# Performance work log

Hardware: AMD Instinct MI355X
Metric: run time of the kernel (lower is better)

The kernel has to match this reference:

```python
import jax, jax.numpy as jnp
import numpy as np

B, S, D_MODEL = 1, 2048, 2048
N_HEADS, N_KV_HEADS, D_HEAD = 16, 4, 128
ROTARY_DIM, ROTARY_BASE = 128, 10000.0
ATTN_SCALE = float(np.sqrt(D_HEAD))
REPEAT = N_HEADS // N_KV_HEADS


def _sin_cos_rotary(n_ctx, rotary_dim, base):
    # TransformerLens calculate_sin_cos_rotary, rotary_adjacent_pairs=False:
    # freq repeated as 'd -> (2 d)'
    pos = jnp.arange(n_ctx, dtype=jnp.float32)
    dim = jnp.arange(rotary_dim // 2, dtype=jnp.float32)
    freq = base ** (dim / (rotary_dim / 2))
    freq = jnp.concatenate([freq, freq])  # (2 d)
    angles = pos[:, None] / freq[None, :]  # [n_ctx, rotary_dim]
    return jnp.sin(angles), jnp.cos(angles)


def _rotate_every_two_half(x):
    # rotate_half for non-adjacent pairs: [-x2, x1]
    d = x.shape[-1]
    return jnp.concatenate([-x[..., d // 2:], x[..., : d // 2]], axis=-1)


def _apply_rotary(x, sin, cos):
    # x: [batch, pos, head, d_head]; sin/cos: [n_ctx, rotary_dim]
    p = x.shape[1]
    s = sin[:p][:, None, :]  # [pos, 1, rotary_dim]
    c = cos[:p][:, None, :]
    x_rot = x[..., :ROTARY_DIM]
    x_pass = x[..., ROTARY_DIM:]
    x_rotated = x_rot * c + _rotate_every_two_half(x_rot) * s
    return jnp.concatenate([x_rotated, x_pass], axis=-1)


def setup_inputs() -> dict:
    key = jax.random.key(0)
    ks = jax.random.split(key, 10)
    init = 1.0 / np.sqrt(D_MODEL)
    return {
        "query_input": jax.random.normal(ks[0], (B, S, D_MODEL), jnp.float32),
        "key_input": jax.random.normal(ks[1], (B, S, D_MODEL), jnp.float32),
        "value_input": jax.random.normal(ks[2], (B, S, D_MODEL), jnp.float32),
        "W_Q": jax.random.normal(ks[3], (N_HEADS, D_MODEL, D_HEAD), jnp.float32) * init,
        "b_Q": jnp.zeros((N_HEADS, D_HEAD), jnp.float32),
        "W_K": jax.random.normal(ks[4], (N_KV_HEADS, D_MODEL, D_HEAD), jnp.float32) * init,
        "b_K": jnp.zeros((N_KV_HEADS, D_HEAD), jnp.float32),
        "W_V": jax.random.normal(ks[5], (N_KV_HEADS, D_MODEL, D_HEAD), jnp.float32) * init,
        "b_V": jnp.zeros((N_KV_HEADS, D_HEAD), jnp.float32),
        "W_O": jax.random.normal(ks[6], (N_HEADS, D_HEAD, D_MODEL), jnp.float32) * init,
        "b_O": jnp.zeros((D_MODEL,), jnp.float32),
    }


def reference(query_input, key_input, value_input, W_Q, b_Q, W_K, b_K, W_V, b_V, W_O, b_O):
    sin, cos = _sin_cos_rotary(S, ROTARY_DIM, ROTARY_BASE)

    # Projections
    q = jnp.einsum("bpd,hdk->bphk", query_input, W_Q) + b_Q   # [B,S,H,dh]
    k = jnp.einsum("bpd,hdk->bphk", key_input, W_K) + b_K     # [B,S,Hkv,dh]
    v = jnp.einsum("bpd,hdk->bphk", value_input, W_V) + b_V   # [B,S,Hkv,dh]

    # Rotary on q and k (before KV head expansion)
    q = _apply_rotary(q, sin, cos)
    k = _apply_rotary(k, sin, cos)

    # GQA expansion via repeat_interleave on head dim
    k = jnp.repeat(k, REPEAT, axis=2)  # [B,S,H,dh]
    v = jnp.repeat(v, REPEAT, axis=2)

    # Attention scores, causal mask, softmax
    scores = jnp.einsum("bqhd,bkhd->bhqk", q, k) / ATTN_SCALE  # [B,H,S,S]
    causal = jnp.tril(jnp.ones((S, S), dtype=bool))
    scores = jnp.where(causal, scores, jnp.finfo(scores.dtype).min)
    pattern = jax.nn.softmax(scores, axis=-1)

    # Weighted values and output projection
    z = jnp.einsum("bhqk,bkhd->bqhd", pattern, v)              # [B,S,H,dh]
    out = jnp.einsum("bqhd,hdm->bqm", z, W_O) + b_O            # [B,S,D]
    return out
```

## Files before the change

### kernel.cpp

```cpp
#include <hip/hip_runtime.h>
#include <hip/hip_bf16.h>
#include <stdint.h>
#include <math.h>

typedef __bf16 bf16_t;
typedef __attribute__((ext_vector_type(8))) __bf16 bf16x8;
typedef __attribute__((ext_vector_type(4))) __bf16 bf16x4;
typedef __attribute__((ext_vector_type(4))) float f32x4;
typedef __attribute__((ext_vector_type(16))) float f32x16;
typedef unsigned int uint2v __attribute__((ext_vector_type(2)));

static constexpr int S = 2048;
static constexpr int DM = 2048;
static constexpr int NH = 16;
static constexpr int NKV = 4;
static constexpr int DH = 128;

#define MFMA16(a, b, c) __builtin_amdgcn_mfma_f32_16x16x32_bf16((a), (b), (c), 0, 0, 0)
#define MFMA32(a, b, c) __builtin_amdgcn_mfma_f32_32x32x16_bf16((a), (b), (c), 0, 0, 0)

__device__ __forceinline__ void gload_lds16(const void* g, void* l) {
  __builtin_amdgcn_global_load_lds((__attribute__((address_space(1))) void*)(g),
                                   (__attribute__((address_space(3))) void*)(l), 16, 0, 0);
}

template <int N>
__device__ __forceinline__ void wait_vmcnt() {
  asm volatile("s_waitcnt vmcnt(%0)" :: "n"(N) : "memory");
}
__device__ __forceinline__ void wait_lgkm0() {
  asm volatile("s_waitcnt lgkmcnt(0)" ::: "memory");
}

__device__ __forceinline__ unsigned cvtpk(float lo, float hi) {
  unsigned r;
  asm("v_cvt_pk_bf16_f32 %0, %1, %2" : "=v"(r) : "v"(lo), "v"(hi));
  return r;
}
__device__ __forceinline__ void plswap2(unsigned& a, unsigned& b) {
  uint2v r = __builtin_amdgcn_permlane32_swap(a, b, false, false);
  a = r[0]; b = r[1];
}
__device__ __forceinline__ float swapred_max(float x) {
  uint2v r = __builtin_amdgcn_permlane32_swap(__float_as_uint(x), __float_as_uint(x), false, false);
  return fmaxf(__uint_as_float(r[0]), __uint_as_float(r[1]));
}
__device__ __forceinline__ float swapred_sum(float x) {
  uint2v r = __builtin_amdgcn_permlane32_swap(__float_as_uint(x), __float_as_uint(x), false, false);
  return __uint_as_float(r[0]) + __uint_as_float(r[1]);
}
__device__ __forceinline__ bf16x8 packfrag(float a0, float a1, float a2, float a3,
                                           float a4, float a5, float a6, float a7) {
  unsigned w0 = cvtpk(a0, a1), w1 = cvtpk(a2, a3);
  unsigned w2 = cvtpk(a4, a5), w3 = cvtpk(a6, a7);
  plswap2(w0, w2); plswap2(w1, w3);
  union { unsigned u[4]; bf16x8 v; } u;
  u.u[0] = w0; u.u[1] = w1; u.u[2] = w2; u.u[3] = w3;
  return u.v;
}

__device__ const unsigned char attn_map[24] = {
  (15<<1)|0,(15<<1)|1,(7<<1)|0,(14<<1)|0,(14<<1)|1,(13<<1)|0,(13<<1)|1,(6<<1)|0,
  (12<<1)|0,(12<<1)|1,(5<<1)|0,(11<<1)|0,(11<<1)|1,(10<<1)|0,(10<<1)|1,(9<<1)|0,
  (9<<1)|1,(4<<1)|0,(8<<1)|0,(8<<1)|1,(3<<1)|0,(2<<1)|0,(1<<1)|0,(0<<1)|0};

__global__ void rope_table_k(float2* __restrict__ tab) {
  int p = blockIdx.x;
  int j = threadIdx.x;
  double inv = exp2(-(double)j * 13.287712379549449 / 64.0);
  double ang = (double)p * inv;
  tab[p * 64 + j] = make_float2((float)sin(ang), (float)cos(ang));
}

__global__ void cvt3_k(const float* __restrict__ Xq, const float* __restrict__ Xk,
                       const float* __restrict__ Xv, bf16_t* __restrict__ xq,
                       bf16_t* __restrict__ xk, bf16_t* __restrict__ xv) {
  int i = (blockIdx.x * 256 + threadIdx.x) * 4;
  const float* in; bf16_t* out; int off;
  if (i < 4194304) { in = Xq; out = xq; off = i; }
  else if (i < 8388608) { in = Xk; out = xk; off = i - 4194304; }
  else { in = Xv; out = xv; off = i - 8388608; }
  f32x4 v = *(const f32x4*)(in + off);
  bf16x4 o;
  o[0] = (bf16_t)v[0]; o[1] = (bf16_t)v[1]; o[2] = (bf16_t)v[2]; o[3] = (bf16_t)v[3];
  *(bf16x4*)(out + off) = o;
}

__global__ void transpose_w_k(const float* __restrict__ in, bf16_t* __restrict__ out,
                              int R, int C, int rb, int cb, int ldo) {
  __shared__ float tile[32][33];
  int b = blockIdx.z;
  int c0 = blockIdx.x * 32, r0 = blockIdx.y * 32;
  int tx = threadIdx.x, ty = threadIdx.y;
  const float* src = in + (size_t)b * R * C;
  #pragma unroll
  for (int j = 0; j < 32; j += 8)
    tile[ty + j][tx] = src[(size_t)(r0 + ty + j) * C + c0 + tx];
  __syncthreads();
  #pragma unroll
  for (int j = 0; j < 32; j += 8) {
    int c = c0 + ty + j;
    int r = r0 + tx;
    out[(size_t)(b * rb + c) * ldo + b * cb + r] = (bf16_t)tile[tx][ty + j];
  }
}

__global__ void transpose_wkv_k(const float* __restrict__ WK, const float* __restrict__ WV,
                                bf16_t* __restrict__ wkT, bf16_t* __restrict__ wvT) {
  __shared__ float tile[32][33];
  int z = blockIdx.z;
  int b = z & 3;
  const float* in = (z < 4) ? WK : WV;
  bf16_t* out = (z < 4) ? wkT : wvT;
  int c0 = blockIdx.x * 32, r0 = blockIdx.y * 32;
  int tx = threadIdx.x, ty = threadIdx.y;
  const float* src = in + (size_t)b * 2048 * 128;
  #pragma unroll
  for (int j = 0; j < 32; j += 8)
    tile[ty + j][tx] = src[(size_t)(r0 + ty + j) * 128 + c0 + tx];
  __syncthreads();
  #pragma unroll
  for (int j = 0; j < 32; j += 8) {
    int c = c0 + ty + j;
    int r = r0 + tx;
    out[(size_t)(b * 128 + c) * 2048 + r] = (bf16_t)tile[tx][ty + j];
  }
}

__global__ void rope_qk_k(bf16_t* __restrict__ Qb, bf16_t* __restrict__ Kb,
                          const float2* __restrict__ tab, float qscale) {
  int tid = blockIdx.x * 256 + threadIdx.x;
  int row = tid >> 4;
  int i = (tid & 15) * 4;
  bf16_t* base; float scale;
  if (row < NH * S) { base = Qb + (size_t)row * DH; scale = qscale; }
  else { base = Kb + (size_t)(row - NH * S) * DH; scale = 1.0f; }
  int p = row & (S - 1);
  bf16x4 lo = *(bf16x4*)(base + i);
  bf16x4 hi = *(bf16x4*)(base + i + 64);
  float4 t0 = *(const float4*)(tab + p * 64 + i);
  float4 t1 = *(const float4*)(tab + p * 64 + i + 2);
  float sv[4] = {t0.x, t0.z, t1.x, t1.z};
  float cv[4] = {t0.y, t0.w, t1.y, t1.w};
  bf16x4 nlo, nhi;
  #pragma unroll
  for (int j = 0; j < 4; ++j) {
    float a = (float)lo[j], b = (float)hi[j];
    nlo[j] = (bf16_t)((a * cv[j] - b * sv[j]) * scale);
    nhi[j] = (bf16_t)((b * cv[j] + a * sv[j]) * scale);
  }
  *(bf16x4*)(base + i) = nlo;
  *(bf16x4*)(base + i + 64) = nhi;
}

__global__ __launch_bounds__(256)
void proj_gemm_k(const bf16_t* __restrict__ xq, const bf16_t* __restrict__ xk,
                 const bf16_t* __restrict__ xv, const bf16_t* __restrict__ wqT,
                 const bf16_t* __restrict__ wkT, const bf16_t* __restrict__ wvT,
                 const float* __restrict__ bQ, const float* __restrict__ bK,
                 const float* __restrict__ bV, bf16_t* __restrict__ Qb,
                 bf16_t* __restrict__ Kb, bf16_t* __restrict__ Vt) {
  const int nb = blockIdx.x;
  const int m0 = blockIdx.y * 128;
  const bf16_t* A; const bf16_t* B; const float* bias; bf16_t* dst; int ncol0;
  bool vmode = false;
  if (nb < 32)      { A = xq; B = wqT; bias = bQ; dst = Qb; ncol0 = nb * 64; }
  else if (nb < 40) { A = xk; B = wkT; bias = bK; dst = Kb; ncol0 = (nb - 32) * 64; }
  else              { A = xv; B = wvT; bias = bV; dst = Vt; ncol0 = (nb - 40) * 64; vmode = true; }
  const int K = 2048;
  const int t = threadIdx.x;
  const int lane = t & 63, w = t >> 6;
  const int l15 = lane & 15, lg = lane >> 4;
  const int wr = (w >> 1) * 64, wc = (w & 1) * 32;

  __shared__ bf16_t lA[2][128 * 64];
  __shared__ bf16_t lB[2][64 * 64];

  f32x4 acc[4][2] = {};
  const int srow = t >> 3;
  const int sslot = t & 7;

  auto stage = [&](int buf, int kt) {
    #pragma unroll
    for (int i = 0; i < 4; ++i) {
      int row = i * 32 + srow;
      int ss = sslot ^ (row & 7);
      gload_lds16(A + (size_t)(m0 + row) * K + kt * 64 + ss * 8,
                  (void*)(&lA[buf][0] + i * 2048 + t * 8));
    }
    #pragma unroll
    for (int i = 0; i < 2; ++i) {
      int row = i * 32 + srow;
      int ss = sslot ^ (row & 7);
      gload_lds16(B + (size_t)(ncol0 + row) * K + kt * 64 + ss * 8,
                  (void*)(&lB[buf][0] + i * 2048 + t * 8));
    }
  };

  const int nk = K >> 6;
  stage(0, 0);
  for (int kt = 0; kt < nk; ++kt) {
    const int cur = kt & 1;
    if (kt + 1 < nk) {
      stage(cur ^ 1, kt + 1);
      wait_vmcnt<6>();
    } else {
      wait_vmcnt<0>();
    }
    __builtin_amdgcn_s_barrier();
    #pragma unroll
    for (int kk = 0; kk < 2; ++kk) {
      bf16x8 af[4], bfv[2];
      #pragma unroll
      for (int f = 0; f < 4; ++f) {
        int row = wr + f * 16 + l15;
        int slot = kk * 4 + lg;
        af[f] = *(const bf16x8*)(&lA[cur][0] + row * 64 + ((slot ^ (row & 7)) * 8));
      }
      #pragma unroll
      for (int f = 0; f < 2; ++f) {
        int row = wc + f * 16 + l15;
        int slot = kk * 4 + lg;
        bfv[f] = *(const bf16x8*)(&lB[cur][0] + row * 64 + ((slot ^ (row & 7)) * 8));
      }
      #pragma unroll
      for (int fm = 0; fm < 4; ++fm)
        #pragma unroll
        for (int fn = 0; fn < 2; ++fn)
          acc[fm][fn] = MFMA16(af[fm], bfv[fn], acc[fm][fn]);
    }
    wait_lgkm0();
    __builtin_amdgcn_s_barrier();
  }

  #pragma unroll
  for (int fm = 0; fm < 4; ++fm) {
    int rowb = m0 + wr + fm * 16 + lg * 4;
    #pragma unroll
    for (int fn = 0; fn < 2; ++fn) {
      int col = ncol0 + wc + fn * 16 + l15;
      float bb = bias[col];
      if (vmode) {
        bf16x4 pk;
        #pragma unroll
        for (int r = 0; r < 4; ++r) pk[r] = (bf16_t)(acc[fm][fn][r] + bb);
        *(bf16x4*)(dst + (size_t)col * S + rowb) = pk;
      } else {
        #pragma unroll
        for (int r = 0; r < 4; ++r) {
          float v = acc[fm][fn][r] + bb;
          dst[((size_t)(col >> 7) * S + (rowb + r)) * DH + (col & 127)] = (bf16_t)v;
        }
      }
    }
  }
}

__global__ __launch_bounds__(256)
void gemm_o_k(const bf16_t* __restrict__ A, const bf16_t* __restrict__ B,
              const float* __restrict__ bias, float* __restrict__ Cout) {
  const int ncol0 = blockIdx.x * 64;
  const int m0 = blockIdx.y * 128;
  const int K = 2048;
  const int t = threadIdx.x;
  const int lane = t & 63, w = t >> 6;
  const int l15 = lane & 15, lg = lane >> 4;
  const int wr = (w >> 1) * 64, wc = (w & 1) * 32;

  __shared__ bf16_t lA[2][128 * 64];
  __shared__ bf16_t lB[2][64 * 64];

  f32x4 acc[4][2] = {};
  const int srow = t >> 3;
  const int sslot = t & 7;

  auto stage = [&](int buf, int kt) {
    #pragma unroll
    for (int i = 0; i < 4; ++i) {
      int row = i * 32 + srow;
      int ss = sslot ^ (row & 7);
      gload_lds16(A + (size_t)(m0 + row) * K + kt * 64 + ss * 8,
                  (void*)(&lA[buf][0] + i * 2048 + t * 8));
    }
    #pragma unroll
    for (int i = 0; i < 2; ++i) {
      int row = i * 32 + srow;
      int ss = sslot ^ (row & 7);
      gload_lds16(B + (size_t)(ncol0 + row) * K + kt * 64 + ss * 8,
                  (void*)(&lB[buf][0] + i * 2048 + t * 8));
    }
  };

  const int nk = K >> 6;
  stage(0, 0);
  for (int kt = 0; kt < nk; ++kt) {
    const int cur = kt & 1;
    if (kt + 1 < nk) {
      stage(cur ^ 1, kt + 1);
      wait_vmcnt<6>();
    } else {
      wait_vmcnt<0>();
    }
    __builtin_amdgcn_s_barrier();
    #pragma unroll
    for (int kk = 0; kk < 2; ++kk) {
      bf16x8 af[4], bfv[2];
      #pragma unroll
      for (int f = 0; f < 4; ++f) {
        int row = wr + f * 16 + l15;
        int slot = kk * 4 + lg;
        af[f] = *(const bf16x8*)(&lA[cur][0] + row * 64 + ((slot ^ (row & 7)) * 8));
      }
      #pragma unroll
      for (int f = 0; f < 2; ++f) {
        int row = wc + f * 16 + l15;
        int slot = kk * 4 + lg;
        bfv[f] = *(const bf16x8*)(&lB[cur][0] + row * 64 + ((slot ^ (row & 7)) * 8));
      }
      #pragma unroll
      for (int fm = 0; fm < 4; ++fm)
        #pragma unroll
        for (int fn = 0; fn < 2; ++fn)
          acc[fm][fn] = MFMA16(af[fm], bfv[fn], acc[fm][fn]);
    }
    wait_lgkm0();
    __builtin_amdgcn_s_barrier();
  }

  #pragma unroll
  for (int fm = 0; fm < 4; ++fm) {
    int rowb = m0 + wr + fm * 16 + lg * 4;
    #pragma unroll
    for (int fn = 0; fn < 2; ++fn) {
      int col = ncol0 + wc + fn * 16 + l15;
      float bb = bias[col];
      #pragma unroll
      for (int r = 0; r < 4; ++r)
        Cout[(size_t)(rowb + r) * DM + col] = acc[fm][fn][r] + bb;
    }
  }
}

__global__ __launch_bounds__(256, 2)
void attn_k(const bf16_t* __restrict__ Q, const bf16_t* __restrict__ K,
            const bf16_t* __restrict__ Vt, bf16_t* __restrict__ Z,
            float* __restrict__ Opart, float* __restrict__ mpart,
            float* __restrict__ lpart) {
  const int bid = blockIdx.x;
  const int h = bid & 15;
  const int g = bid >> 4;
  const int code = attn_map[g];
  const int qb = code >> 1, ci = code & 1;
  const bool split = qb >= 8;
  const int kt0 = (split && ci) ? (qb + 1) : 0;
  const int ktend = split ? (ci ? 2 * qb + 1 : qb) : 2 * qb + 1;
  const int q0 = qb * 128;
  const int hkv = h >> 2;
  const int t = threadIdx.x;
  const int lane = t & 63, w = t >> 6;
  const int l31 = lane & 31, hi = lane >> 5;
  const int qrow = q0 + w * 32 + l31;

  __shared__ bf16_t lK[2][64 * 128];
  __shared__ bf16_t lV[2][128 * 64];

  bf16x8 qf[8];
  #pragma unroll
  for (int j = 0; j < 8; ++j)
    qf[j] = *(const bf16x8*)(Q + ((size_t)h * S + qrow) * DH + j * 16 + hi * 8);

  auto stageKV = [&](int buf, int kt) {
    #pragma unroll
    for (int i = 0; i < 4; ++i) {
      int row = i * 16 + (t >> 4);
      int ss = (t & 15) ^ (row & 15);
      gload_lds16(K + ((size_t)hkv * S + kt * 64 + row) * DH + ss * 8,
                  (void*)(&lK[buf][0] + i * 2048 + t * 8));
    }
    #pragma unroll
    for (int i = 0; i < 4; ++i) {
      int row = i * 32 + (t >> 3);
      int ss = (t & 7) ^ (row & 7);
      gload_lds16(Vt + ((size_t)hkv * DH + row) * S + kt * 64 + ss * 8,
                  (void*)(&lV[buf][0] + i * 2048 + t * 8));
    }
  };

  f32x16 oacc0 = {}, oacc1 = {}, oacc2 = {}, oacc3 = {};
  float m_run = -3.0e3f, l_run = 0.f;

  stageKV(0, kt0);
  for (int kt = kt0; kt <= ktend; ++kt) {
    const int cur = (kt - kt0) & 1;
    if (kt < ktend) {
      stageKV(cur ^ 1, kt + 1);
      wait_vmcnt<8>();
    } else {
      wait_vmcnt<0>();
    }
    __builtin_amdgcn_s_barrier();

    f32x16 s0 = {}, s1 = {};
    __builtin_amdgcn_s_setprio(1);
    #pragma unroll
    for (int j = 0; j < 8; ++j) {
      int sIdx = j * 2 + hi;
      int r0 = l31;
      bf16x8 k0 = *(const bf16x8*)(&lK[cur][0] + r0 * 128 + ((sIdx ^ (r0 & 15)) * 8));
      s0 = MFMA32(k0, qf[j], s0);
      int r1 = 32 + l31;
      bf16x8 k1 = *(const bf16x8*)(&lK[cur][0] + r1 * 128 + ((sIdx ^ (r1 & 15)) * 8));
      s1 = MFMA32(k1, qf[j], s1);
    }
    __builtin_amdgcn_s_setprio(0);

    if (kt >= 2 * qb) {
      #pragma unroll
      for (int r = 0; r < 16; ++r) {
        int krow = kt * 64 + (r & 3) + 8 * (r >> 2) + 4 * hi;
        if (krow > qrow) s0[r] = -1e30f;
        if (krow + 32 > qrow) s1[r] = -1e30f;
      }
    }

    float mxa = s0[0], mxb = s0[1], mxc = s0[2], mxd = s0[3];
    #pragma unroll
    for (int r = 4; r < 16; r += 4) {
      mxa = fmaxf(mxa, s0[r]); mxb = fmaxf(mxb, s0[r + 1]);
      mxc = fmaxf(mxc, s0[r + 2]); mxd = fmaxf(mxd, s0[r + 3]);
    }
    #pragma unroll
    for (int r = 0; r < 16; r += 4) {
      mxa = fmaxf(mxa, s1[r]); mxb = fmaxf(mxb, s1[r + 1]);
      mxc = fmaxf(mxc, s1[r + 2]); mxd = fmaxf(mxd, s1[r + 3]);
    }
    float mfull = swapred_max(fmaxf(fmaxf(mxa, mxb), fmaxf(mxc, mxd)));

    float m_new, alpha;
    bool nore = __all(mfull - m_run <= 8.0f);
    if (nore) { m_new = m_run; alpha = 1.0f; }
    else { m_new = fmaxf(m_run, mfull); alpha = exp2f(m_run - m_new); }

    float psa = 0.f, psb = 0.f, psc = 0.f, psd = 0.f;
    #pragma unroll
    for (int r = 0; r < 16; r += 4) {
      s0[r] = exp2f(s0[r] - m_new); psa += s0[r];
      s0[r + 1] = exp2f(s0[r + 1] - m_new); psb += s0[r + 1];
      s0[r + 2] = exp2f(s0[r + 2] - m_new); psc += s0[r + 2];
      s0[r + 3] = exp2f(s0[r + 3] - m_new); psd += s0[r + 3];
    }
    #pragma unroll
    for (int r = 0; r < 16; r += 4) {
      s1[r] = exp2f(s1[r] - m_new); psa += s1[r];
      s1[r + 1] = exp2f(s1[r + 1] - m_new); psb += s1[r + 1];
      s1[r + 2] = exp2f(s1[r + 2] - m_new); psc += s1[r + 2];
      s1[r + 3] = exp2f(s1[r + 3] - m_new); psd += s1[r + 3];
    }
    float lt = swapred_sum((psa + psb) + (psc + psd));
    l_run = l_run * alpha + lt;
    m_run = m_new;

    if (!nore) {
      #pragma unroll
      for (int r = 0; r < 16; ++r) {
        int qs = (r & 3) + 8 * (r >> 2) + 4 * hi;
        float ar = __shfl(alpha, qs);
        oacc0[r] *= ar; oacc1[r] *= ar; oacc2[r] *= ar; oacc3[r] *= ar;
      }
    }

    bf16x8 pa[4];
    pa[0] = packfrag(s0[0], s0[1], s0[2], s0[3], s0[4], s0[5], s0[6], s0[7]);
    pa[1] = packfrag(s0[8], s0[9], s0[10], s0[11], s0[12], s0[13], s0[14], s0[15]);
    pa[2] = packfrag(s1[0], s1[1], s1[2], s1[3], s1[4], s1[5], s1[6], s1[7]);
    pa[3] = packfrag(s1[8], s1[9], s1[10], s1[11], s1[12], s1[13], s1[14], s1[15]);

    __builtin_amdgcn_s_setprio(1);
#define PVBLK(OA, db) { \
    int dr = (db) * 32 + l31; \
    _Pragma("unroll") \
    for (int ks = 0; ks < 4; ++ks) { \
      int sIdx = ks * 2 + hi; \
      bf16x8 vf = *(const bf16x8*)(&lV[cur][0] + dr * 64 + ((sIdx ^ (dr & 7)) * 8)); \
      OA = MFMA32(pa[ks], vf, OA); \
    } }
    PVBLK(oacc0, 0)
    PVBLK(oacc1, 1)
    PVBLK(oacc2, 2)
    PVBLK(oacc3, 3)
#undef PVBLK
    __builtin_amdgcn_s_setprio(0);
    wait_lgkm0();
    __builtin_amdgcn_s_barrier();
  }

  if (!split) {
    float linv = 1.0f / l_run;
    #pragma unroll
    for (int r = 0; r < 16; ++r) {
      int qs = (r & 3) + 8 * (r >> 2) + 4 * hi;
      float lv = __shfl(linv, qs);
      int qg = q0 + w * 32 + qs;
      bf16_t* zp = Z + (size_t)qg * DM + h * DH + l31;
      zp[0]  = (bf16_t)(oacc0[r] * lv);
      zp[32] = (bf16_t)(oacc1[r] * lv);
      zp[64] = (bf16_t)(oacc2[r] * lv);
      zp[96] = (bf16_t)(oacc3[r] * lv);
    }
  } else {
    const int slot = (h * 8 + (qb - 8)) * 2 + ci;
    float* Op = Opart + (size_t)slot * 16384;
    #pragma unroll
    for (int r = 0; r < 16; ++r) {
      int qs = (r & 3) + 8 * (r >> 2) + 4 * hi;
      float* op = Op + (w * 32 + qs) * 128 + l31;
      op[0] = oacc0[r]; op[32] = oacc1[r]; op[64] = oacc2[r]; op[96] = oacc3[r];
    }
    if (lane < 32) {
      mpart[slot * 128 + w * 32 + l31] = m_run;
      lpart[slot * 128 + w * 32 + l31] = l_run;
    }
  }
}

__global__ void combine_k(const float* __restrict__ Opart, const float* __restrict__ mpart,
                          const float* __restrict__ lpart, bf16_t* __restrict__ Z) {
  int tid = blockIdx.x * 256 + threadIdx.x;
  int d = tid & 127;
  int q = (tid >> 7) & 127;
  int qb8 = (tid >> 14) & 7;
  int h = tid >> 17;
  int s0 = (h * 8 + qb8) * 2;
  float m0 = mpart[s0 * 128 + q], m1 = mpart[(s0 + 1) * 128 + q];
  float l0 = lpart[s0 * 128 + q], l1 = lpart[(s0 + 1) * 128 + q];
  float M = fmaxf(m0, m1);
  float a0 = exp2f(m0 - M), a1 = exp2f(m1 - M);
  float L = a0 * l0 + a1 * l1;
  float o0 = Opart[(size_t)s0 * 16384 + q * 128 + d];
  float o1 = Opart[(size_t)(s0 + 1) * 16384 + q * 128 + d];
  int qg = (8 + qb8) * 128 + q;
  Z[(size_t)qg * DM + h * DH + d] = (bf16_t)((a0 * o0 + a1 * o1) / L);
}

extern "C" void kernel_launch(void* const* d_in, const int* in_sizes, int n_in,
                              void* d_out, int out_size, void* d_ws, size_t ws_size,
                              hipStream_t stream) {
  (void)in_sizes; (void)n_in; (void)out_size; (void)ws_size;
  const float* Xq = (const float*)d_in[0];
  const float* Xk = (const float*)d_in[1];
  const float* Xv = (const float*)d_in[2];
  const float* WQ = (const float*)d_in[3];
  const float* bQ = (const float*)d_in[4];
  const float* WK = (const float*)d_in[5];
  const float* bK = (const float*)d_in[6];
  const float* WV = (const float*)d_in[7];
  const float* bV = (const float*)d_in[8];
  const float* WO = (const float*)d_in[9];
  const float* bO = (const float*)d_in[10];

  char* w = (char*)d_ws;
  float2* tab = (float2*)w;
  bf16_t* xq  = (bf16_t*)(w + (1 << 20));
  bf16_t* xk  = xq + 4194304;
  bf16_t* xv  = xk + 4194304;
  bf16_t* wqT = xv + 4194304;
  bf16_t* wkT = wqT + 4194304;
  bf16_t* wvT = wkT + 1048576;
  bf16_t* woT = wvT + 1048576;
  bf16_t* Qb  = woT + 4194304;
  bf16_t* Kb  = Qb + 4194304;
  bf16_t* Vtb = Kb + 1048576;
  bf16_t* Zb  = Vtb + 1048576;
  float* Opart = (float*)xq;
  float* mpart = (float*)xv;
  float* lpart = mpart + 256 * 128;

  rope_table_k<<<dim3(S), dim3(64), 0, stream>>>(tab);
  cvt3_k<<<dim3(12288), dim3(256), 0, stream>>>(Xq, Xk, Xv, xq, xk, xv);
  transpose_w_k<<<dim3(4, 64, 16), dim3(32, 8), 0, stream>>>(WQ, wqT, 2048, 128, 128, 0, 2048);
  transpose_wkv_k<<<dim3(4, 64, 8), dim3(32, 8), 0, stream>>>(WK, WV, wkT, wvT);
  transpose_w_k<<<dim3(64, 4, 16), dim3(32, 8), 0, stream>>>(WO, woT, 128, 2048, 0, 128, 2048);

  proj_gemm_k<<<dim3(48, 16), dim3(256), 0, stream>>>(xq, xk, xv, wqT, wkT, wvT,
                                                      bQ, bK, bV, Qb, Kb, Vtb);

  const float qscale = 1.4426950408889634f / sqrtf(128.0f);
  rope_qk_k<<<dim3(2560), dim3(256), 0, stream>>>(Qb, Kb, tab, qscale);

  attn_k<<<dim3(384), dim3(256), 0, stream>>>(Qb, Kb, Vtb, Zb, Opart, mpart, lpart);
  combine_k<<<dim3(8192), dim3(256), 0, stream>>>(Opart, mpart, lpart, Zb);

  gemm_o_k<<<dim3(32, 16), dim3(256), 0, stream>>>(Zb, woT, bO, (float*)d_out);
}
```

Measured before the change: 157.5 us.

## Split attention KV range into 10-tile chunks and load K fragments directly from global

Changes the causal attention work split from at most two halves per query block to chunks of 10 KV tiles. This raises the grid from 384 to 544 blocks and evens out per-block work. The combine kernel now merges a variable number of partials. K fragments are read straight from global/L2 into registers instead of being staged through LDS, which halves LDS use and moves the barrier to just before the PV stage. In exchange, there are more partial writes and combine traffic, and the uncached global K reads may add latency to the QK^T stage.

```diff
diff --git a/kernel.cpp b/kernel.cpp
--- a/kernel.cpp
+++ b/kernel.cpp
@@ -59,10 +59,10 @@
   return u.v;
 }
 
-__device__ const unsigned char attn_map[24] = {
-  (15<<1)|0,(15<<1)|1,(7<<1)|0,(14<<1)|0,(14<<1)|1,(13<<1)|0,(13<<1)|1,(6<<1)|0,
-  (12<<1)|0,(12<<1)|1,(5<<1)|0,(11<<1)|0,(11<<1)|1,(10<<1)|0,(10<<1)|1,(9<<1)|0,
-  (9<<1)|1,(4<<1)|0,(8<<1)|0,(8<<1)|1,(3<<1)|0,(2<<1)|0,(1<<1)|0,(0<<1)|0};
+__device__ const unsigned char attn_map[34] = {
+  60, 61, 62, 56, 57, 58, 52, 53, 48, 49, 44, 45, 40, 41, 36, 37, 32,
+  28, 24, 20, 16, 12, 33, 54, 8, 29, 50, 4, 25, 46, 0, 21, 42, 63};
+__device__ const unsigned char sbase[16] = {0,0,0,0,0, 0,2,4,6,8, 10,13,16,19,22, 25};
 
 __global__ void rope_table_k(float2* __restrict__ tab) {
   int p = blockIdx.x;
@@ -350,10 +350,11 @@
   const int h = bid & 15;
   const int g = bid >> 4;
   const int code = attn_map[g];
-  const int qb = code >> 1, ci = code & 1;
-  const bool split = qb >= 8;
-  const int kt0 = (split && ci) ? (qb + 1) : 0;
-  const int ktend = split ? (ci ? 2 * qb + 1 : qb) : 2 * qb + 1;
+  const int qb = code >> 2, ci = code & 3;
+  const int ntiles = 2 * qb + 2;
+  const bool split = ntiles > 10;
+  const int kt0 = 10 * ci;
+  const int ktend = min(10 * ci + 9, 2 * qb + 1);
   const int q0 = qb * 128;
   const int hkv = h >> 2;
   const int t = threadIdx.x;
@@ -361,7 +362,6 @@
   const int l31 = lane & 31, hi = lane >> 5;
   const int qrow = q0 + w * 32 + l31;
 
-  __shared__ bf16_t lK[2][64 * 128];
   __shared__ bf16_t lV[2][128 * 64];
 
   bf16x8 qf[8];
@@ -369,14 +369,7 @@
   for (int j = 0; j < 8; ++j)
     qf[j] = *(const bf16x8*)(Q + ((size_t)h * S + qrow) * DH + j * 16 + hi * 8);
 
-  auto stageKV = [&](int buf, int kt) {
-    #pragma unroll
-    for (int i = 0; i < 4; ++i) {
-      int row = i * 16 + (t >> 4);
-      int ss = (t & 15) ^ (row & 15);
-      gload_lds16(K + ((size_t)hkv * S + kt * 64 + row) * DH + ss * 8,
-                  (void*)(&lK[buf][0] + i * 2048 + t * 8));
-    }
+  auto stageV = [&](int buf, int kt) {
     #pragma unroll
     for (int i = 0; i < 4; ++i) {
       int row = i * 32 + (t >> 3);
@@ -389,27 +382,19 @@
   f32x16 oacc0 = {}, oacc1 = {}, oacc2 = {}, oacc3 = {};
   float m_run = -3.0e3f, l_run = 0.f;
 
-  stageKV(0, kt0);
+  stageV(0, kt0);
   for (int kt = kt0; kt <= ktend; ++kt) {
     const int cur = (kt - kt0) & 1;
-    if (kt < ktend) {
-      stageKV(cur ^ 1, kt + 1);
-      wait_vmcnt<8>();
-    } else {
-      wait_vmcnt<0>();
-    }
-    __builtin_amdgcn_s_barrier();
-
+    if (kt < ktend) stageV(cur ^ 1, kt + 1);
+
+    const bf16_t* kp = K + ((size_t)hkv * S + (size_t)kt * 64 + l31) * DH + hi * 8;
     f32x16 s0 = {}, s1 = {};
     __builtin_amdgcn_s_setprio(1);
     #pragma unroll
     for (int j = 0; j < 8; ++j) {
-      int sIdx = j * 2 + hi;
-      int r0 = l31;
-      bf16x8 k0 = *(const bf16x8*)(&lK[cur][0] + r0 * 128 + ((sIdx ^ (r0 & 15)) * 8));
+      bf16x8 k0 = *(const bf16x8*)(kp + j * 16);
+      bf16x8 k1 = *(const bf16x8*)(kp + 32 * DH + j * 16);
       s0 = MFMA32(k0, qf[j], s0);
-      int r1 = 32 + l31;
-      bf16x8 k1 = *(const bf16x8*)(&lK[cur][0] + r1 * 128 + ((sIdx ^ (r1 & 15)) * 8));
       s1 = MFMA32(k1, qf[j], s1);
     }
     __builtin_amdgcn_s_setprio(0);
@@ -474,6 +459,9 @@
     pa[1] = packfrag(s0[8], s0[9], s0[10], s0[11], s0[12], s0[13], s0[14], s0[15]);
     pa[2] = packfrag(s1[0], s1[1], s1[2], s1[3], s1[4], s1[5], s1[6], s1[7]);
     pa[3] = packfrag(s1[8], s1[9], s1[10], s1[11], s1[12], s1[13], s1[14], s1[15]);
+
+    wait_vmcnt<0>();
+    __builtin_amdgcn_s_barrier();
 
     __builtin_amdgcn_s_setprio(1);
 #define PVBLK(OA, db) { \
@@ -508,7 +496,7 @@
       zp[96] = (bf16_t)(oacc3[r] * lv);
     }
   } else {
-    const int slot = (h * 8 + (qb - 8)) * 2 + ci;
+    const int slot = h * 29 + sbase[qb] + ci;
     float* Op = Opart + (size_t)slot * 16384;
     #pragma unroll
     for (int r = 0; r < 16; ++r) {
@@ -528,18 +516,23 @@
   int tid = blockIdx.x * 256 + threadIdx.x;
   int d = tid & 127;
   int q = (tid >> 7) & 127;
-  int qb8 = (tid >> 14) & 7;
-  int h = tid >> 17;
-  int s0 = (h * 8 + qb8) * 2;
-  float m0 = mpart[s0 * 128 + q], m1 = mpart[(s0 + 1) * 128 + q];
-  float l0 = lpart[s0 * 128 + q], l1 = lpart[(s0 + 1) * 128 + q];
-  float M = fmaxf(m0, m1);
-  float a0 = exp2f(m0 - M), a1 = exp2f(m1 - M);
-  float L = a0 * l0 + a1 * l1;
-  float o0 = Opart[(size_t)s0 * 16384 + q * 128 + d];
-  float o1 = Opart[(size_t)(s0 + 1) * 16384 + q * 128 + d];
-  int qg = (8 + qb8) * 128 + q;
-  Z[(size_t)qg * DM + h * DH + d] = (bf16_t)((a0 * o0 + a1 * o1) / L);
+  int u = tid >> 14;
+  int h = u / 11;
+  int qb = 5 + (u - h * 11);
+  int nc = (2 * qb + 11) / 10;
+  int slot0 = h * 29 + sbase[qb];
+  float M = -3.0e3f;
+  #pragma unroll 4
+  for (int c = 0; c < nc; ++c) M = fmaxf(M, mpart[(slot0 + c) * 128 + q]);
+  float L = 0.f, O = 0.f;
+  #pragma unroll 4
+  for (int c = 0; c < nc; ++c) {
+    float a = exp2f(mpart[(slot0 + c) * 128 + q] - M);
+    L += a * lpart[(slot0 + c) * 128 + q];
+    O += a * Opart[(size_t)(slot0 + c) * 16384 + q * 128 + d];
+  }
+  int qg = qb * 128 + q;
+  Z[(size_t)qg * DM + h * DH + d] = (bf16_t)(O / L);
 }
 
 extern "C" void kernel_launch(void* const* d_in, const int* in_sizes, int n_in,
@@ -572,8 +565,8 @@
   bf16_t* Vtb = Kb + 1048576;
   bf16_t* Zb  = Vtb + 1048576;
   float* Opart = (float*)xq;
-  float* mpart = (float*)xv;
-  float* lpart = mpart + 256 * 128;
+  float* mpart = (float*)wkT;
+  float* lpart = mpart + 464 * 128;
 
   rope_table_k<<<dim3(S), dim3(64), 0, stream>>>(tab);
   cvt3_k<<<dim3(12288), dim3(256), 0, stream>>>(Xq, Xk, Xv, xq, xk, xv);
@@ -587,8 +580,8 @@
   const float qscale = 1.4426950408889634f / sqrtf(128.0f);
   rope_qk_k<<<dim3(2560), dim3(256), 0, stream>>>(Qb, Kb, tab, qscale);
 
-  attn_k<<<dim3(384), dim3(256), 0, stream>>>(Qb, Kb, Vtb, Zb, Opart, mpart, lpart);
-  combine_k<<<dim3(8192), dim3(256), 0, stream>>>(Opart, mpart, lpart, Zb);
+  attn_k<<<dim3(544), dim3(256), 0, stream>>>(Qb, Kb, Vtb, Zb, Opart, mpart, lpart);
+  combine_k<<<dim3(11264), dim3(256), 0, stream>>>(Opart, mpart, lpart, Zb);
 
   gemm_o_k<<<dim3(32, 16), dim3(256), 0, stream>>>(Zb, woT, bO, (float*)d_out);
 }
```

Measured after the change: 182.0 us. +15.6%, slower.

## Split attention into fixed 5-tile KV chunks, merge prep kernels, bf16 partials

Applied to the files above, without the earlier changes.

Attention work is now divided into chunks of at most five KV tiles per block, so 976 blocks of roughly equal size replace 384 blocks that were unbalanced under the causal mask. The combine kernel merges a variable number of partial results per query block and works on four elements per thread. Partial outputs are stored in bf16 to halve that traffic, and the rope table, conversion and transpose kernels are fused into one prep launch to cut launch overhead. The costs are more partial-result traffic and combine work, plus some precision loss in the partials. The m/l partials now reuse the rope table buffer, which is overwritten only after rope_qk has run.

```diff
diff --git a/kernel.cpp b/kernel.cpp
--- a/kernel.cpp
+++ b/kernel.cpp
@@ -59,71 +59,80 @@
   return u.v;
 }
 
-__device__ const unsigned char attn_map[24] = {
-  (15<<1)|0,(15<<1)|1,(7<<1)|0,(14<<1)|0,(14<<1)|1,(13<<1)|0,(13<<1)|1,(6<<1)|0,
-  (12<<1)|0,(12<<1)|1,(5<<1)|0,(11<<1)|0,(11<<1)|1,(10<<1)|0,(10<<1)|1,(9<<1)|0,
-  (9<<1)|1,(4<<1)|0,(8<<1)|0,(8<<1)|1,(3<<1)|0,(2<<1)|0,(1<<1)|0,(0<<1)|0};
-
-__global__ void rope_table_k(float2* __restrict__ tab) {
-  int p = blockIdx.x;
-  int j = threadIdx.x;
-  double inv = exp2(-(double)j * 13.287712379549449 / 64.0);
-  double ang = (double)p * inv;
-  tab[p * 64 + j] = make_float2((float)sin(ang), (float)cos(ang));
-}
-
-__global__ void cvt3_k(const float* __restrict__ Xq, const float* __restrict__ Xk,
-                       const float* __restrict__ Xv, bf16_t* __restrict__ xq,
-                       bf16_t* __restrict__ xk, bf16_t* __restrict__ xv) {
-  int i = (blockIdx.x * 256 + threadIdx.x) * 4;
-  const float* in; bf16_t* out; int off;
-  if (i < 4194304) { in = Xq; out = xq; off = i; }
-  else if (i < 8388608) { in = Xk; out = xk; off = i - 4194304; }
-  else { in = Xv; out = xv; off = i - 8388608; }
-  f32x4 v = *(const f32x4*)(in + off);
-  bf16x4 o;
-  o[0] = (bf16_t)v[0]; o[1] = (bf16_t)v[1]; o[2] = (bf16_t)v[2]; o[3] = (bf16_t)v[3];
-  *(bf16x4*)(out + off) = o;
-}
-
-__global__ void transpose_w_k(const float* __restrict__ in, bf16_t* __restrict__ out,
-                              int R, int C, int rb, int cb, int ldo) {
+__device__ const unsigned char attn_map[61] = {
+  120,121,122,123,124,125,126, 112,113,114,115,116,117, 104,105,106,107,108,109,
+  96,97,98,99,100,101, 88,89,90,91,92, 80,81,82,83,84, 72,73,74,75, 64,65,66,67,
+  56,57,58,59, 48,49,50, 40,41,42, 32,33, 24,25, 16,17, 8, 0};
+__device__ const unsigned char sbase[16] = {0,0,0,2,4,6,9,12,16,20,24,29,34,40,46,52};
+
+__global__ __launch_bounds__(256)
+void prep_k(const float* __restrict__ Xq, const float* __restrict__ Xk,
+            const float* __restrict__ Xv, const float* __restrict__ WQ,
+            const float* __restrict__ WK, const float* __restrict__ WV,
+            const float* __restrict__ WO, float2* __restrict__ tab,
+            bf16_t* __restrict__ xq, bf16_t* __restrict__ xk, bf16_t* __restrict__ xv,
+            bf16_t* __restrict__ wqT, bf16_t* __restrict__ wkT, bf16_t* __restrict__ wvT,
+            bf16_t* __restrict__ woT) {
   __shared__ float tile[32][33];
-  int b = blockIdx.z;
-  int c0 = blockIdx.x * 32, r0 = blockIdx.y * 32;
-  int tx = threadIdx.x, ty = threadIdx.y;
-  const float* src = in + (size_t)b * R * C;
-  #pragma unroll
-  for (int j = 0; j < 32; j += 8)
-    tile[ty + j][tx] = src[(size_t)(r0 + ty + j) * C + c0 + tx];
-  __syncthreads();
-  #pragma unroll
-  for (int j = 0; j < 32; j += 8) {
-    int c = c0 + ty + j;
-    int r = r0 + tx;
-    out[(size_t)(b * rb + c) * ldo + b * cb + r] = (bf16_t)tile[tx][ty + j];
-  }
-}
-
-__global__ void transpose_wkv_k(const float* __restrict__ WK, const float* __restrict__ WV,
-                                bf16_t* __restrict__ wkT, bf16_t* __restrict__ wvT) {
-  __shared__ float tile[32][33];
-  int z = blockIdx.z;
-  int b = z & 3;
-  const float* in = (z < 4) ? WK : WV;
-  bf16_t* out = (z < 4) ? wkT : wvT;
-  int c0 = blockIdx.x * 32, r0 = blockIdx.y * 32;
-  int tx = threadIdx.x, ty = threadIdx.y;
-  const float* src = in + (size_t)b * 2048 * 128;
-  #pragma unroll
-  for (int j = 0; j < 32; j += 8)
-    tile[ty + j][tx] = src[(size_t)(r0 + ty + j) * 128 + c0 + tx];
-  __syncthreads();
-  #pragma unroll
-  for (int j = 0; j < 32; j += 8) {
-    int c = c0 + ty + j;
-    int r = r0 + tx;
-    out[(size_t)(b * 128 + c) * 2048 + r] = (bf16_t)tile[tx][ty + j];
+  const int b = blockIdx.x, t = threadIdx.x;
+  if (b < 512) {
+    int idx = b * 256 + t;
+    int p = idx >> 6, j = idx & 63;
+    double inv = exp2(-(double)j * 13.287712379549449 / 64.0);
+    double ang = (double)p * inv;
+    tab[idx] = make_float2((float)sin(ang), (float)cos(ang));
+  } else if (b < 12800) {
+    int i = ((b - 512) * 256 + t) * 4;
+    const float* in; bf16_t* out; int off;
+    if (i < 4194304) { in = Xq; out = xq; off = i; }
+    else if (i < 8388608) { in = Xk; out = xk; off = i - 4194304; }
+    else { in = Xv; out = xv; off = i - 8388608; }
+    f32x4 v = *(const f32x4*)(in + off);
+    bf16x4 o;
+    o[0] = (bf16_t)v[0]; o[1] = (bf16_t)v[1]; o[2] = (bf16_t)v[2]; o[3] = (bf16_t)v[3];
+    *(bf16x4*)(out + off) = o;
+  } else if (b < 16896) {
+    int b2 = b - 12800;
+    int bx = b2 & 3, by = (b2 >> 2) & 63, bz = b2 >> 8;
+    int c0 = bx * 32, r0 = by * 32;
+    int tx = t & 31, ty = t >> 5;
+    const float* src = WQ + (size_t)bz * 2048 * 128;
+    #pragma unroll
+    for (int j = 0; j < 32; j += 8)
+      tile[ty + j][tx] = src[(size_t)(r0 + ty + j) * 128 + c0 + tx];
+    __syncthreads();
+    #pragma unroll
+    for (int j = 0; j < 32; j += 8)
+      wqT[(size_t)(bz * 128 + c0 + ty + j) * 2048 + r0 + tx] = (bf16_t)tile[tx][ty + j];
+  } else if (b < 18944) {
+    int b2 = b - 16896;
+    int bx = b2 & 3, by = (b2 >> 2) & 63, bz = b2 >> 8;
+    int g = bz & 3;
+    const float* in = (bz < 4) ? WK : WV;
+    bf16_t* out = (bz < 4) ? wkT : wvT;
+    int c0 = bx * 32, r0 = by * 32;
+    int tx = t & 31, ty = t >> 5;
+    const float* src = in + (size_t)g * 2048 * 128;
+    #pragma unroll
+    for (int j = 0; j < 32; j += 8)
+      tile[ty + j][tx] = src[(size_t)(r0 + ty + j) * 128 + c0 + tx];
+    __syncthreads();
+    #pragma unroll
+    for (int j = 0; j < 32; j += 8)
+      out[(size_t)(g * 128 + c0 + ty + j) * 2048 + r0 + tx] = (bf16_t)tile[tx][ty + j];
+  } else {
+    int b2 = b - 18944;
+    int bx = b2 & 63, by = (b2 >> 6) & 3, bz = b2 >> 8;
+    int c0 = bx * 32, r0 = by * 32;
+    int tx = t & 31, ty = t >> 5;
+    const float* src = WO + (size_t)bz * 128 * 2048;
+    #pragma unroll
+    for (int j = 0; j < 32; j += 8)
+      tile[ty + j][tx] = src[(size_t)(r0 + ty + j) * 2048 + c0 + tx];
+    __syncthreads();
+    #pragma unroll
+    for (int j = 0; j < 32; j += 8)
+      woT[(size_t)(c0 + ty + j) * 2048 + bz * 128 + r0 + tx] = (bf16_t)tile[tx][ty + j];
   }
 }
 
@@ -344,16 +353,17 @@
 __global__ __launch_bounds__(256, 2)
 void attn_k(const bf16_t* __restrict__ Q, const bf16_t* __restrict__ K,
             const bf16_t* __restrict__ Vt, bf16_t* __restrict__ Z,
-            float* __restrict__ Opart, float* __restrict__ mpart,
+            bf16_t* __restrict__ Opart, float* __restrict__ mpart,
             float* __restrict__ lpart) {
   const int bid = blockIdx.x;
   const int h = bid & 15;
   const int g = bid >> 4;
   const int code = attn_map[g];
-  const int qb = code >> 1, ci = code & 1;
-  const bool split = qb >= 8;
-  const int kt0 = (split && ci) ? (qb + 1) : 0;
-  const int ktend = split ? (ci ? 2 * qb + 1 : qb) : 2 * qb + 1;
+  const int qb = code >> 3, ci = code & 7;
+  const bool split = qb >= 2;
+  const int kt0 = 5 * ci;
+  const int kteA = 5 * ci + 4, kteB = 2 * qb + 1;
+  const int ktend = kteA < kteB ? kteA : kteB;
   const int q0 = qb * 128;
   const int hkv = h >> 2;
   const int t = threadIdx.x;
@@ -508,13 +518,16 @@
       zp[96] = (bf16_t)(oacc3[r] * lv);
     }
   } else {
-    const int slot = (h * 8 + (qb - 8)) * 2 + ci;
-    float* Op = Opart + (size_t)slot * 16384;
+    const int slot = h * 59 + sbase[qb] + ci;
+    bf16_t* Op = Opart + (size_t)slot * 16384;
     #pragma unroll
     for (int r = 0; r < 16; ++r) {
       int qs = (r & 3) + 8 * (r >> 2) + 4 * hi;
-      float* op = Op + (w * 32 + qs) * 128 + l31;
-      op[0] = oacc0[r]; op[32] = oacc1[r]; op[64] = oacc2[r]; op[96] = oacc3[r];
+      bf16_t* op = Op + (w * 32 + qs) * 128 + l31;
+      op[0]  = (bf16_t)oacc0[r];
+      op[32] = (bf16_t)oacc1[r];
+      op[64] = (bf16_t)oacc2[r];
+      op[96] = (bf16_t)oacc3[r];
     }
     if (lane < 32) {
       mpart[slot * 128 + w * 32 + l31] = m_run;
@@ -523,23 +536,33 @@
   }
 }
 
-__global__ void combine_k(const float* __restrict__ Opart, const float* __restrict__ mpart,
+__global__ void combine_k(const bf16_t* __restrict__ Opart, const float* __restrict__ mpart,
                           const float* __restrict__ lpart, bf16_t* __restrict__ Z) {
   int tid = blockIdx.x * 256 + threadIdx.x;
-  int d = tid & 127;
-  int q = (tid >> 7) & 127;
-  int qb8 = (tid >> 14) & 7;
-  int h = tid >> 17;
-  int s0 = (h * 8 + qb8) * 2;
-  float m0 = mpart[s0 * 128 + q], m1 = mpart[(s0 + 1) * 128 + q];
-  float l0 = lpart[s0 * 128 + q], l1 = lpart[(s0 + 1) * 128 + q];
-  float M = fmaxf(m0, m1);
-  float a0 = exp2f(m0 - M), a1 = exp2f(m1 - M);
-  float L = a0 * l0 + a1 * l1;
-  float o0 = Opart[(size_t)s0 * 16384 + q * 128 + d];
-  float o1 = Opart[(size_t)(s0 + 1) * 16384 + q * 128 + d];
-  int qg = (8 + qb8) * 128 + q;
-  Z[(size_t)qg * DM + h * DH + d] = (bf16_t)((a0 * o0 + a1 * o1) / L);
+  int d4 = tid & 31;
+  int q = (tid >> 5) & 127;
+  int u = tid >> 12;
+  int h = u / 14;
+  int qb = 2 + (u - h * 14);
+  int nc = (2 * qb + 6) / 5;
+  int slot0 = h * 59 + sbase[qb];
+  float M = -3.0e3f;
+  for (int c = 0; c < nc; ++c) M = fmaxf(M, mpart[(slot0 + c) * 128 + q]);
+  float L = 0.f;
+  float o0 = 0.f, o1 = 0.f, o2 = 0.f, o3 = 0.f;
+  for (int c = 0; c < nc; ++c) {
+    float a = exp2f(mpart[(slot0 + c) * 128 + q] - M);
+    L += a * lpart[(slot0 + c) * 128 + q];
+    bf16x4 ov = *(const bf16x4*)(Opart + (size_t)(slot0 + c) * 16384 + q * 128 + d4 * 4);
+    o0 += a * (float)ov[0]; o1 += a * (float)ov[1];
+    o2 += a * (float)ov[2]; o3 += a * (float)ov[3];
+  }
+  float inv = 1.0f / L;
+  bf16x4 zv;
+  zv[0] = (bf16_t)(o0 * inv); zv[1] = (bf16_t)(o1 * inv);
+  zv[2] = (bf16_t)(o2 * inv); zv[3] = (bf16_t)(o3 * inv);
+  int qg = qb * 128 + q;
+  *(bf16x4*)(Z + (size_t)qg * DM + h * DH + d4 * 4) = zv;
 }
 
 extern "C" void kernel_launch(void* const* d_in, const int* in_sizes, int n_in,
@@ -571,15 +594,12 @@
   bf16_t* Kb  = Qb + 4194304;
   bf16_t* Vtb = Kb + 1048576;
   bf16_t* Zb  = Vtb + 1048576;
-  float* Opart = (float*)xq;
-  float* mpart = (float*)xv;
-  float* lpart = mpart + 256 * 128;
-
-  rope_table_k<<<dim3(S), dim3(64), 0, stream>>>(tab);
-  cvt3_k<<<dim3(12288), dim3(256), 0, stream>>>(Xq, Xk, Xv, xq, xk, xv);
-  transpose_w_k<<<dim3(4, 64, 16), dim3(32, 8), 0, stream>>>(WQ, wqT, 2048, 128, 128, 0, 2048);
-  transpose_wkv_k<<<dim3(4, 64, 8), dim3(32, 8), 0, stream>>>(WK, WV, wkT, wvT);
-  transpose_w_k<<<dim3(64, 4, 16), dim3(32, 8), 0, stream>>>(WO, woT, 128, 2048, 0, 128, 2048);
+  bf16_t* Opart = xq;
+  float* mpart = (float*)tab;
+  float* lpart = mpart + 944 * 128;
+
+  prep_k<<<dim3(23040), dim3(256), 0, stream>>>(Xq, Xk, Xv, WQ, WK, WV, WO, tab,
+                                                xq, xk, xv, wqT, wkT, wvT, woT);
 
   proj_gemm_k<<<dim3(48, 16), dim3(256), 0, stream>>>(xq, xk, xv, wqT, wkT, wvT,
                                                       bQ, bK, bV, Qb, Kb, Vtb);
@@ -587,8 +607,8 @@
   const float qscale = 1.4426950408889634f / sqrtf(128.0f);
   rope_qk_k<<<dim3(2560), dim3(256), 0, stream>>>(Qb, Kb, tab, qscale);
 
-  attn_k<<<dim3(384), dim3(256), 0, stream>>>(Qb, Kb, Vtb, Zb, Opart, mpart, lpart);
-  combine_k<<<dim3(8192), dim3(256), 0, stream>>>(Opart, mpart, lpart, Zb);
+  attn_k<<<dim3(976), dim3(256), 0, stream>>>(Qb, Kb, Vtb, Zb, Opart, mpart, lpart);
+  combine_k<<<dim3(3584), dim3(256), 0, stream>>>(Opart, mpart, lpart, Zb);
 
   gemm_o_k<<<dim3(32, 16), dim3(256), 0, stream>>>(Zb, woT, bO, (float*)d_out);
 }
```

New measurement: 149.2 us. 1.06x faster.
